# Kernel optimization log

Hardware: AMD Instinct MI355X
Metric: run time of the kernel (lower is better)

The kernel has to match this reference:

```python
import jax, jax.numpy as jnp
import numpy as np

N_NODES = 100000
N_EDGES = 640000
HIDDEN = 128


def setup_inputs() -> dict:
    key = jax.random.key(0)
    k_h, k_e, k_w1, k_b1, k_w2, k_b2 = jax.random.split(key, 6)
    h = jax.random.normal(k_h, (N_NODES, HIDDEN), dtype=jnp.float32)
    edge_index = jax.random.randint(k_e, (2, N_EDGES), 0, N_NODES, dtype=jnp.int64)
    # nn.Linear default init: U(-1/sqrt(fan_in), 1/sqrt(fan_in))
    lim1 = 1.0 / np.sqrt(2 * HIDDEN)
    W1 = jax.random.uniform(k_w1, (2 * HIDDEN, HIDDEN), jnp.float32, -lim1, lim1)
    b1 = jax.random.uniform(k_b1, (HIDDEN,), jnp.float32, -lim1, lim1)
    lim2 = 1.0 / np.sqrt(HIDDEN)
    W2 = jax.random.uniform(k_w2, (HIDDEN, 1), jnp.float32, -lim2, lim2)
    b2 = jax.random.uniform(k_b2, (1,), jnp.float32, -lim2, lim2)
    return {"h": h, "edge_index": edge_index, "W1": W1, "b1": b1, "W2": W2, "b2": b2}


def reference(h, edge_index, W1, b1, W2, b2):
    src, dst = edge_index[0], edge_index[1]
    # cat([h[src], h[dst]]) @ W1 == h[src] @ W1[:H] + h[dst] @ W1[H:]
    W1s, W1d = W1[:HIDDEN], W1[HIDDEN:]
    x = h[src] @ W1s + h[dst] @ W1d + b1          # [E, H]
    x = jax.nn.relu(x)
    score = x @ W2 + b2                            # [E, 1]
    return score.squeeze(-1)                       # [E]
```

## Files before the change

kernel.cpp:

```cpp
#include <hip/hip_runtime.h>

#define HIDDEN 128

typedef _Float16 f16x8 __attribute__((ext_vector_type(8)));
typedef _Float16 f16x4 __attribute__((ext_vector_type(4)));
typedef _Float16 f16x2 __attribute__((ext_vector_type(2)));
typedef float f32x4 __attribute__((ext_vector_type(4)));

__global__ __launch_bounds__(64) void prep_w(const float* __restrict__ W1,
                                             _Float16* __restrict__ Wpk) {
  const int blk = blockIdx.x;
  const int jt = blk >> 2;
  const int kt = blk & 3;
  const int lane = threadIdx.x;
  const int col = jt * 16 + (lane & 15);
  const int kbase = kt * 32 + (lane >> 4) * 8;
  f16x8 v;
#pragma unroll
  for (int j = 0; j < 8; ++j) {
    const int k = kbase + j;
    const float w = (col < HIDDEN) ? W1[k * HIDDEN + col]
                                   : W1[(HIDDEN + k) * HIDDEN + (col - HIDDEN)];
    v[j] = (_Float16)w;
  }
  *reinterpret_cast<f16x8*>(Wpk + ((size_t)blk * 64 + lane) * 8) = v;
}

__global__ __launch_bounds__(256, 3) void gemm_mfma_v4(
    const float* __restrict__ h, const _Float16* __restrict__ Wpk,
    const float* __restrict__ b1, _Float16* __restrict__ Af,
    _Float16* __restrict__ Bf, int n_nodes, int ntiles) {
  const int lane = threadIdx.x & 63;
  const int wave = threadIdx.x >> 6;
  const int nl = lane & 15;
  const int kgrp = lane >> 4;
  const int jt0 = wave * 4;

  const f16x8* wp = reinterpret_cast<const f16x8*>(Wpk);
  f16x8 wfrag[4][4];
#pragma unroll
  for (int j4 = 0; j4 < 4; ++j4)
#pragma unroll
    for (int kt = 0; kt < 4; ++kt)
      wfrag[j4][kt] = wp[((jt0 + j4) * 4 + kt) * 64 + lane];

  f32x4 binit[4];
#pragma unroll
  for (int j4 = 0; j4 < 4; ++j4) {
    const int jt = jt0 + j4;
    if (jt < 8) {
      binit[j4] = *reinterpret_cast<const f32x4*>(b1 + jt * 16 + kgrp * 4);
    } else {
      binit[j4][0] = 0.f; binit[j4][1] = 0.f; binit[j4][2] = 0.f; binit[j4][3] = 0.f;
    }
  }

  float4 buf[8];
  f16x8 hfrag[4];

  auto LOAD = [&](int tile) {
    int node = tile * 16 + nl;
    if (node >= n_nodes) node = 0;
    const float4* hp = reinterpret_cast<const float4*>(h) +
                       (size_t)node * 32 + kgrp * 2;
#pragma unroll
    for (int kt = 0; kt < 4; ++kt) {
      buf[kt * 2]     = hp[kt * 8];
      buf[kt * 2 + 1] = hp[kt * 8 + 1];
    }
  };

  auto CVT = [&]() {
#pragma unroll
    for (int kt = 0; kt < 4; ++kt) {
      const float4 v0 = buf[kt * 2];
      const float4 v1 = buf[kt * 2 + 1];
      hfrag[kt][0] = (_Float16)v0.x; hfrag[kt][1] = (_Float16)v0.y;
      hfrag[kt][2] = (_Float16)v0.z; hfrag[kt][3] = (_Float16)v0.w;
      hfrag[kt][4] = (_Float16)v1.x; hfrag[kt][5] = (_Float16)v1.y;
      hfrag[kt][6] = (_Float16)v1.z; hfrag[kt][7] = (_Float16)v1.w;
    }
  };

  auto COMPUTE_STORE = [&](int tile) {
    f32x4 acc[4];
#pragma unroll
    for (int j4 = 0; j4 < 4; ++j4) acc[j4] = binit[j4];
#pragma unroll
    for (int kt = 0; kt < 4; ++kt)
#pragma unroll
      for (int j4 = 0; j4 < 4; ++j4)
        acc[j4] = __builtin_amdgcn_mfma_f32_16x16x32_f16(
            wfrag[j4][kt], hfrag[kt], acc[j4], 0, 0, 0);
    const int node = tile * 16 + nl;
    if (node < n_nodes) {
#pragma unroll
      for (int j4 = 0; j4 < 4; ++j4) {
        const int jt = jt0 + j4;
        _Float16* dst = ((jt < 8) ? Af : Bf) +
                        (size_t)node * HIDDEN + (jt & 7) * 16 + kgrp * 4;
        f16x4 v;
        v[0] = (_Float16)acc[j4][0];
        v[1] = (_Float16)acc[j4][1];
        v[2] = (_Float16)acc[j4][2];
        v[3] = (_Float16)acc[j4][3];
        *reinterpret_cast<f16x4*>(dst) = v;
      }
    }
  };

  const int stride = gridDim.x;
  int tile = blockIdx.x;
  if (tile >= ntiles) return;

  LOAD(tile);
  CVT();
  int next = tile + stride;
  if (next < ntiles) LOAD(next);

  while (true) {
    COMPUTE_STORE(tile);
    if (next >= ntiles) break;
    CVT();
    const int next2 = next + stride;
    if (next2 < ntiles) LOAD(next2);
    tile = next;
    next = next2;
  }
}

__global__ __launch_bounds__(256) void edge_score_v3(
    const int* __restrict__ ei, const _Float16* __restrict__ Af,
    const _Float16* __restrict__ Bf, const float* __restrict__ W2,
    const float* __restrict__ b2, float* __restrict__ out, int n_edges) {
  const int wid = (int)((blockIdx.x * 256 + threadIdx.x) >> 6);
  const int lane = threadIdx.x & 63;
  const int e0 = wid * 16;
  if (e0 >= n_edges) return;

  int srcs[16], dsts[16];
#pragma unroll
  for (int k = 0; k < 16; ++k) {
    srcs[k] = ei[e0 + k];
    dsts[k] = ei[n_edges + e0 + k];
  }

  f16x2 av[16], bv[16];
#pragma unroll
  for (int k = 0; k < 16; ++k)
    av[k] = reinterpret_cast<const f16x2*>(Af + (size_t)srcs[k] * HIDDEN)[lane];
#pragma unroll
  for (int k = 0; k < 16; ++k)
    bv[k] = reinterpret_cast<const f16x2*>(Bf + (size_t)dsts[k] * HIDDEN)[lane];

  const float2 w2v = reinterpret_cast<const float2*>(W2)[lane];
  float p[16];
#pragma unroll
  for (int k = 0; k < 16; ++k) {
    float x0 = (float)av[k][0] + (float)bv[k][0];
    float x1 = (float)av[k][1] + (float)bv[k][1];
    x0 = fmaxf(x0, 0.f);
    x1 = fmaxf(x1, 0.f);
    p[k] = fmaf(x0, w2v.x, x1 * w2v.y);
  }

  auto mrg = [&](float a, float b, int off) {
    const float as = a + __shfl_xor(a, off, 64);
    const float bs = b + __shfl_xor(b, off, 64);
    return (lane & off) ? bs : as;
  };
  float q[8];
#pragma unroll
  for (int i = 0; i < 8; ++i) q[i] = mrg(p[2 * i], p[2 * i + 1], 1);
  float r[4];
#pragma unroll
  for (int i = 0; i < 4; ++i) r[i] = mrg(q[2 * i], q[2 * i + 1], 2);
  float s2[2];
#pragma unroll
  for (int i = 0; i < 2; ++i) s2[i] = mrg(r[2 * i], r[2 * i + 1], 4);
  float t = mrg(s2[0], s2[1], 8);
  t += __shfl_xor(t, 16, 64);
  t += __shfl_xor(t, 32, 64);

  if (lane < 16 && e0 + lane < n_edges) out[e0 + lane] = t + b2[0];
}

__global__ __launch_bounds__(256) void fused_fallback(
    const float* __restrict__ h, const int* __restrict__ ei,
    const float* __restrict__ W1, const float* __restrict__ b1,
    const float* __restrict__ W2, const float* __restrict__ b2,
    float* __restrict__ out, int n_edges) {
  const int e = (int)((blockIdx.x * 256 + threadIdx.x) >> 6);
  const int lane = threadIdx.x & 63;
  if (e >= n_edges) return;
  const int src = ei[e], dst = ei[n_edges + e];
  const float* hs = h + (size_t)src * HIDDEN;
  const float* hd = h + (size_t)dst * HIDDEN;
  float acc0 = b1[lane], acc1 = b1[lane + 64];
  for (int k = 0; k < HIDDEN; ++k) {
    const float s = hs[k], d = hd[k];
    acc0 = fmaf(s, W1[k * HIDDEN + lane], acc0);
    acc0 = fmaf(d, W1[(k + HIDDEN) * HIDDEN + lane], acc0);
    acc1 = fmaf(s, W1[k * HIDDEN + lane + 64], acc1);
    acc1 = fmaf(d, W1[(k + HIDDEN) * HIDDEN + lane + 64], acc1);
  }
  acc0 = acc0 > 0.f ? acc0 : 0.f;
  acc1 = acc1 > 0.f ? acc1 : 0.f;
  float p = fmaf(acc0, W2[lane], acc1 * W2[lane + 64]);
#pragma unroll
  for (int off = 32; off >= 1; off >>= 1) p += __shfl_down(p, off, 64);
  if (lane == 0) out[e] = p + b2[0];
}

extern "C" void kernel_launch(void* const* d_in, const int* in_sizes, int n_in,
                              void* d_out, int out_size, void* d_ws, size_t ws_size,
                              hipStream_t stream) {
  const float* h  = (const float*)d_in[0];
  const int*   ei = (const int*)d_in[1];
  const float* W1 = (const float*)d_in[2];
  const float* b1 = (const float*)d_in[3];
  const float* W2 = (const float*)d_in[4];
  const float* b2 = (const float*)d_in[5];
  float* out = (float*)d_out;

  const int n_nodes = in_sizes[0] / HIDDEN;
  const int n_edges = in_sizes[1] / 2;

  const size_t wpk_halfs  = 64 * 64 * 8;
  const size_t proj_halfs = (size_t)n_nodes * HIDDEN;
  const size_t need = (wpk_halfs + 2 * proj_halfs) * sizeof(_Float16);

  if (ws_size >= need) {
    _Float16* Wpk = (_Float16*)d_ws;
    _Float16* A   = Wpk + wpk_halfs;
    _Float16* B   = A + proj_halfs;

    prep_w<<<64, 64, 0, stream>>>(W1, Wpk);

    const int ntiles = (n_nodes + 15) / 16;
    const int gblocks = ntiles < 768 ? ntiles : 768;
    gemm_mfma_v4<<<gblocks, 256, 0, stream>>>(h, Wpk, b1, A, B, n_nodes, ntiles);

    const int nwaves = (n_edges + 15) / 16;
    const int eblocks = (nwaves + 3) / 4;
    edge_score_v3<<<eblocks, 256, 0, stream>>>(ei, A, B, W2, b2, out, n_edges);
  } else {
    const int eblocks = (n_edges + 3) / 4;
    fused_fallback<<<eblocks, 256, 0, stream>>>(h, ei, W1, b1, W2, b2, out, n_edges);
  }
}
```

Baseline: 93.20 us.

## Raise GEMM occupancy, pack f16 conversions, and use fp16 dot in edge scoring

Result: slower. 154.7 us (+66.0%).

```diff
diff --git a/kernel.cpp b/kernel.cpp
--- a/kernel.cpp
+++ b/kernel.cpp
@@ -5,6 +5,7 @@
 typedef _Float16 f16x8 __attribute__((ext_vector_type(8)));
 typedef _Float16 f16x4 __attribute__((ext_vector_type(4)));
 typedef _Float16 f16x2 __attribute__((ext_vector_type(2)));
+typedef __fp16   fp16v2 __attribute__((ext_vector_type(2)));
 typedef float f32x4 __attribute__((ext_vector_type(4)));
 
 __global__ __launch_bounds__(64) void prep_w(const float* __restrict__ W1,
@@ -26,7 +27,7 @@
   *reinterpret_cast<f16x8*>(Wpk + ((size_t)blk * 64 + lane) * 8) = v;
 }
 
-__global__ __launch_bounds__(256, 3) void gemm_mfma_v4(
+__global__ __launch_bounds__(256, 5) void gemm_mfma_v5(
     const float* __restrict__ h, const _Float16* __restrict__ Wpk,
     const float* __restrict__ b1, _Float16* __restrict__ Af,
     _Float16* __restrict__ Bf, int n_nodes, int ntiles) {
@@ -75,10 +76,14 @@
     for (int kt = 0; kt < 4; ++kt) {
       const float4 v0 = buf[kt * 2];
       const float4 v1 = buf[kt * 2 + 1];
-      hfrag[kt][0] = (_Float16)v0.x; hfrag[kt][1] = (_Float16)v0.y;
-      hfrag[kt][2] = (_Float16)v0.z; hfrag[kt][3] = (_Float16)v0.w;
-      hfrag[kt][4] = (_Float16)v1.x; hfrag[kt][5] = (_Float16)v1.y;
-      hfrag[kt][6] = (_Float16)v1.z; hfrag[kt][7] = (_Float16)v1.w;
+      const fp16v2 p0 = __builtin_amdgcn_cvt_pkrtz(v0.x, v0.y);
+      const fp16v2 p1 = __builtin_amdgcn_cvt_pkrtz(v0.z, v0.w);
+      const fp16v2 p2 = __builtin_amdgcn_cvt_pkrtz(v1.x, v1.y);
+      const fp16v2 p3 = __builtin_amdgcn_cvt_pkrtz(v1.z, v1.w);
+      hfrag[kt][0] = (_Float16)p0[0]; hfrag[kt][1] = (_Float16)p0[1];
+      hfrag[kt][2] = (_Float16)p1[0]; hfrag[kt][3] = (_Float16)p1[1];
+      hfrag[kt][4] = (_Float16)p2[0]; hfrag[kt][5] = (_Float16)p2[1];
+      hfrag[kt][6] = (_Float16)p3[0]; hfrag[kt][7] = (_Float16)p3[1];
     }
   };
 
@@ -129,7 +134,7 @@
   }
 }
 
-__global__ __launch_bounds__(256) void edge_score_v3(
+__global__ __launch_bounds__(256) void edge_score_v4(
     const int* __restrict__ ei, const _Float16* __restrict__ Af,
     const _Float16* __restrict__ Bf, const float* __restrict__ W2,
     const float* __restrict__ b2, float* __restrict__ out, int n_edges) {
@@ -145,23 +150,33 @@
     dsts[k] = ei[n_edges + e0 + k];
   }
 
+  const char* Afc = (const char*)Af;
+  const char* Bfc = (const char*)Bf;
+  const unsigned int loff = (unsigned int)(lane << 2);
+
   f16x2 av[16], bv[16];
 #pragma unroll
-  for (int k = 0; k < 16; ++k)
-    av[k] = reinterpret_cast<const f16x2*>(Af + (size_t)srcs[k] * HIDDEN)[lane];
-#pragma unroll
-  for (int k = 0; k < 16; ++k)
-    bv[k] = reinterpret_cast<const f16x2*>(Bf + (size_t)dsts[k] * HIDDEN)[lane];
+  for (int k = 0; k < 16; ++k) {
+    const unsigned int off = ((unsigned int)srcs[k] << 8) + loff;
+    av[k] = *reinterpret_cast<const f16x2*>(Afc + off);
+  }
+#pragma unroll
+  for (int k = 0; k < 16; ++k) {
+    const unsigned int off = ((unsigned int)dsts[k] << 8) + loff;
+    bv[k] = *reinterpret_cast<const f16x2*>(Bfc + off);
+  }
 
   const float2 w2v = reinterpret_cast<const float2*>(W2)[lane];
+  const fp16v2 w2h = __builtin_amdgcn_cvt_pkrtz(w2v.x, w2v.y);
+  const _Float16 h0 = (_Float16)0.f;
+
   float p[16];
 #pragma unroll
   for (int k = 0; k < 16; ++k) {
-    float x0 = (float)av[k][0] + (float)bv[k][0];
-    float x1 = (float)av[k][1] + (float)bv[k][1];
-    x0 = fmaxf(x0, 0.f);
-    x1 = fmaxf(x1, 0.f);
-    p[k] = fmaf(x0, w2v.x, x1 * w2v.y);
+    f16x2 s = av[k] + bv[k];
+    s[0] = s[0] > h0 ? s[0] : h0;
+    s[1] = s[1] > h0 ? s[1] : h0;
+    p[k] = __builtin_amdgcn_fdot2(__builtin_bit_cast(fp16v2, s), w2h, 0.f, false);
   }
 
   auto mrg = [&](float a, float b, int off) {
@@ -238,12 +253,12 @@
     prep_w<<<64, 64, 0, stream>>>(W1, Wpk);
 
     const int ntiles = (n_nodes + 15) / 16;
-    const int gblocks = ntiles < 768 ? ntiles : 768;
-    gemm_mfma_v4<<<gblocks, 256, 0, stream>>>(h, Wpk, b1, A, B, n_nodes, ntiles);
+    const int gblocks = ntiles < 1280 ? ntiles : 1280;
+    gemm_mfma_v5<<<gblocks, 256, 0, stream>>>(h, Wpk, b1, A, B, n_nodes, ntiles);
 
     const int nwaves = (n_edges + 15) / 16;
     const int eblocks = (nwaves + 3) / 4;
-    edge_score_v3<<<eblocks, 256, 0, stream>>>(ei, A, B, W2, b2, out, n_edges);
+    edge_score_v4<<<eblocks, 256, 0, stream>>>(ei, A, B, W2, b2, out, n_edges);
   } else {
     const int eblocks = (n_edges + 3) / 4;
     fused_fallback<<<eblocks, 256, 0, stream>>>(h, ei, W1, b1, W2, b2, out, n_edges);
```
